# Kernel optimization log

Measured on AMD Instinct MI355X. Metric: run time of the kernel, lower is better.

## Reference

```python
import jax, jax.numpy as jnp
import numpy as np

P = 3  # patchsize
EMB = 1024  # pretrain/target embed dimension


def adaptive_avg_pool1d(x, T):
    """torch.F.adaptive_avg_pool1d over last axis (static boundaries)."""
    L = x.shape[-1]
    i = np.arange(T)
    starts = (i * L) // T
    ends = -((-(i + 1) * L) // T)  # ceil((i+1)*L/T)
    cs = jnp.cumsum(x, axis=-1)
    cs = jnp.concatenate([jnp.zeros(x.shape[:-1] + (1,), x.dtype), cs], axis=-1)
    return (cs[..., ends] - cs[..., starts]) / jnp.asarray(ends - starts, x.dtype)


def patchify(x):
    """nn.Unfold(kernel=3, stride=1, pad=1): [B,C,H,W] -> [B,H*W,C,3,3]."""
    B, C, H, W = x.shape
    xp = jnp.pad(x, ((0, 0), (0, 0), (1, 1), (1, 1)))
    pats = jnp.stack([xp[:, :, i:i + H, j:j + W] for i in range(P) for j in range(P)], axis=2)
    pats = pats.reshape(B, C, P, P, H * W).transpose(0, 4, 1, 2, 3)
    return pats, (H, W)


def embed(feat2, feat3):
    B = feat2.shape[0]
    f2, (h0, w0) = patchify(feat2)   # [B, h0*w0, 512, 3, 3]
    f3, (h1, w1) = patchify(feat3)   # [B, h1*w1, 1024, 3, 3]
    C3 = feat3.shape[1]
    # align layer3 patch grid to layer2 grid (bilinear, align_corners=False)
    f3 = f3.reshape(B, h1, w1, C3, P, P).transpose(0, 3, 4, 5, 1, 2)
    f3 = f3.reshape(-1, h1, w1)
    f3 = jax.image.resize(f3, (f3.shape[0], h0, w0), method='bilinear')
    f3 = f3.reshape(B, C3, P, P, h0, w0).transpose(0, 4, 5, 1, 2, 3)
    f3 = f3.reshape(B, h0 * w0, C3, P, P)
    # Preprocessing: MeanMapper per layer -> [N, 2, 1024]
    feats = []
    for f in (f2, f3):
        flat = f.reshape(-1, 1, f.shape[-3] * P * P)       # [N, 1, C*9]
        feats.append(adaptive_avg_pool1d(flat, EMB)[:, 0, :])
    x = jnp.stack(feats, axis=1)                           # [N, 2, 1024]
    # Aggregator: adaptive pool over flattened [N, 1, 2048] -> [N, 1024]
    x = adaptive_avg_pool1d(x.reshape(x.shape[0], 1, -1), EMB)[:, 0, :]
    return x, (h0, w0)


def setup_inputs() -> dict:
    key = jax.random.key(0)
    k1, k2, k3 = jax.random.split(key, 3)
    feat2 = jax.random.normal(k1, (8, 512, 28, 28), dtype=jnp.float32)
    feat3 = jax.random.normal(k2, (8, 1024, 14, 14), dtype=jnp.float32)
    memory_bank = jax.random.normal(k3, (16384, 1024), dtype=jnp.float32)
    return {"feat2": feat2, "feat3": feat3, "memory_bank": memory_bank}


def reference(feat2, feat3, memory_bank):
    B = feat2.shape[0]
    q, (h0, w0) = embed(feat2, feat3)                      # [B*h0*w0, 1024]
    # squared-L2 1-NN against the memory bank (faiss IndexFlatL2, k=1)
    d2 = (jnp.sum(q * q, axis=-1, keepdims=True)
          - 2.0 * (q @ memory_bank.T)
          + jnp.sum(memory_bank * memory_bank, axis=-1)[None, :])
    patch_scores = jnp.min(d2, axis=-1).reshape(B, h0, w0)  # unpatch_scores
    image_scores = jnp.max(patch_scores.reshape(B, -1), axis=-1)  # PatchMaker.score
    return image_scores, patch_scores
```

## Files before the change

### kernel.cpp

```cpp
#include <hip/hip_runtime.h>
#include <hip/hip_bf16.h>

typedef signed char i8;
typedef unsigned char u8;
typedef unsigned short u16;
typedef unsigned int u32;
typedef __attribute__((ext_vector_type(4))) int i32x4;

#define GLD16(g, l) __builtin_amdgcn_global_load_lds((const __attribute__((address_space(1))) u32*)(g), (__attribute__((address_space(3))) u32*)(l), 16, 0, 0)

#define SB (4.5f / 127.f)
#define SQ (2.0f / 127.f)
#define INV_SB (127.f / 4.5f)
#define INV_SQ (127.f / 2.0f)
#define TWO_S (2.0f * SB * SQ)

__device__ __forceinline__ u32 flipf(float f) {
    u32 u = __float_as_uint(f);
    return (u >> 31) ? ~u : (u | 0x80000000u);
}

__device__ __forceinline__ float unflipf(u32 k) {
    return __uint_as_float((k >> 31) ? (k ^ 0x80000000u) : ~k);
}

__device__ __forceinline__ int q8(float x, float invs) {
    return __float2int_rn(fminf(fmaxf(x * invs, -127.f), 127.f));
}

__device__ __forceinline__ void taps(int o, int& i0, int& i1, float& w0, float& w1) {
    int k = (o - 1) >> 1;
    float fy = (0.5f * (float)o - 0.25f) - (float)k;
    i0 = k; i1 = k + 1;
    w0 = 1.0f - fy; w1 = fy;
    if (i0 < 0)  { i0 = 0;  w0 = 0.0f; w1 = 1.0f; }
    if (i1 > 13) { i1 = 13; w1 = 0.0f; w0 = 1.0f; }
}

__global__ __launch_bounds__(256) void u_init_kernel(
    const float* __restrict__ f3, float* __restrict__ U,
    u32* __restrict__ minkey, float* __restrict__ qn2) {
    int bid = blockIdx.x, tid = threadIdx.x;
    if (bid < 25) {
        int i = bid * 256 + tid;
        if (i < 6400) minkey[i] = 0xFFFFFFFFu;
        if (i < 6272) qn2[i] = 0.f;
    }
    int idx = bid * 256 + tid;
    if (idx >= 8 * 512 * 196) return;
    int b = idx / (512 * 196);
    int rem = idx % (512 * 196);
    int t = rem / 196;
    int yx = rem % 196;
    int y = yx / 14, x = yx % 14;
    const float* p0 = f3 + ((size_t)(b * 1024 + 2 * t)) * 196;
    const float* p1 = p0 + 196;
    float s = 0.f;
    #pragma unroll
    for (int dy = -1; dy <= 1; ++dy) {
        int yy = y + dy; if ((unsigned)yy >= 14u) continue;
        #pragma unroll
        for (int dx = -1; dx <= 1; ++dx) {
            int xx = x + dx; if ((unsigned)xx >= 14u) continue;
            s += p0[yy * 14 + xx] + p1[yy * 14 + xx];
        }
    }
    U[idx] = s;
}

__global__ __launch_bounds__(256) void mbq_kernel(
    const float* __restrict__ mb, u8* __restrict__ mbb, float* __restrict__ mb2,
    const float* __restrict__ feat2, const float* __restrict__ U,
    u8* __restrict__ qb, float* __restrict__ qn2) {
    __shared__ float lds[3 * 64 * 29];
    const int bid0 = blockIdx.x;
    const int tid = threadIdx.x;

    if (bid0 >= 3584) {
        const int mrow = bid0 - 3584;
        float4 v = ((const float4*)(mb + (size_t)mrow * 1024))[tid];
        u32 p = ((u32)(u8)(i8)q8(v.x, INV_SB))
              | ((u32)(u8)(i8)q8(v.y, INV_SB) << 8)
              | ((u32)(u8)(i8)q8(v.z, INV_SB) << 16)
              | ((u32)(u8)(i8)q8(v.w, INV_SB) << 24);
        ((u32*)(mbb + (size_t)mrow * 1024))[tid] = p;
        float ssq = v.x * v.x + v.y * v.y + v.z * v.z + v.w * v.w;
        for (int s = 32; s; s >>= 1) ssq += __shfl_down(ssq, s);
        if ((tid & 63) == 0) lds[tid >> 6] = ssq;
        __syncthreads();
        if (tid == 0) mb2[mrow] = lds[0] + lds[1] + lds[2] + lds[3];
        return;
    }

    const int bid = bid0;
    const int b = bid / (28 * 16);
    const int rem = bid % (28 * 16);
    const int h = rem / 16;
    const int chunk = rem % 16;
    const int lane = tid & 63;
    const int wg = tid >> 6;

    if (chunk < 8) {
        const int c0 = chunk * 64;
        for (int i = tid; i < 3 * 64 * 28; i += 256) {
            int r = i / 1792;
            int rr = i % 1792;
            int c = rr / 28, x = rr % 28;
            int y = h - 1 + r;
            lds[(r * 64 + c) * 29 + x] = ((unsigned)y < 28u)
                ? feat2[((size_t)(b * 512 + c0 + c) * 28 + y) * 28 + x] : 0.f;
        }
        __syncthreads();
        const float* rowp = &lds[lane * 29];
        #pragma unroll
        for (int wi = 0; wi < 7; ++wi) {
            const int w = wg * 7 + wi;
            float s = 0.f;
            #pragma unroll
            for (int r = 0; r < 3; ++r) {
                #pragma unroll
                for (int dx = -1; dx <= 1; ++dx) {
                    int x = w + dx;
                    if ((unsigned)x >= 28u) continue;
                    float wt = (r == 1 && dx == 0) ? 2.f : 1.f;
                    s += wt * rowp[r * 64 * 29 + x];
                }
            }
            float val = s * 0.1f;
            const int n = b * 784 + h * 28 + w;
            qb[(size_t)n * 1024 + c0 + lane] = (u8)(i8)q8(val, INV_SQ);
            float ss = val * val;
            for (int sft = 32; sft; sft >>= 1) ss += __shfl_down(ss, sft);
            if (lane == 0) atomicAdd(&qn2[n], ss);
        }
    } else {
        const int t0 = (chunk - 8) * 64;
        int y0, y1; float wy0, wy1;
        taps(h, y0, y1, wy0, wy1);
        for (int i = tid; i < 2 * 64 * 14; i += 256) {
            int r = i / 896;
            int rr = i % 896;
            int t = rr / 14, x = rr % 14;
            lds[(r * 64 + t) * 15 + x] =
                U[(size_t)(b * 512 + t0 + t) * 196 + (r ? y1 : y0) * 14 + x];
        }
        __syncthreads();
        const float* rp0 = &lds[lane * 15];
        const float* rp1 = &lds[(64 + lane) * 15];
        #pragma unroll
        for (int wi = 0; wi < 7; ++wi) {
            const int w = wg * 7 + wi;
            int x0, x1; float wx0, wx1;
            taps(w, x0, x1, wx0, wx1);
            float val = (wy0 * (wx0 * rp0[x0] + wx1 * rp0[x1])
                       + wy1 * (wx0 * rp1[x0] + wx1 * rp1[x1])) * (1.f / 18.f);
            const int n = b * 784 + h * 28 + w;
            qb[(size_t)n * 1024 + 512 + t0 + lane] = (u8)(i8)q8(val, INV_SQ);
            float ss = val * val;
            for (int sft = 32; sft; sft >>= 1) ss += __shfl_down(ss, sft);
            if (lane == 0) atomicAdd(&qn2[n], ss);
        }
    }
}

__global__ __launch_bounds__(512, 4) void gemm_min_kernel(
    const u8* __restrict__ qb, const u8* __restrict__ mbb,
    const float* __restrict__ qn2, const float* __restrict__ mb2,
    u32* __restrict__ minkeys) {
    __shared__ __align__(16) u8 As[2][8192];
    __shared__ __align__(16) u8 Bs[2][16384];
    __shared__ u32 rowmin[128];

    const int tid = threadIdx.x;
    const int wid = tid >> 6;
    const int lane = tid & 63;
    const int wm = wid >> 2;
    const int wn = wid & 3;

    const int flat = blockIdx.x;
    const int swz = (flat & 7) * 400 + (flat >> 3);
    const int q0 = (swz % 50) * 128;
    const int m0 = (swz / 50) * 256;

    const int rloc = wid * 16 + (lane >> 2);
    const int sslot = (lane & 3) ^ ((lane >> 3) & 3);
    const size_t gA  = (size_t)(q0 + rloc) * 1024 + sslot * 16;
    const size_t gB0 = (size_t)(m0 + rloc) * 1024 + sslot * 16;
    const size_t gB1 = (size_t)(m0 + 128 + rloc) * 1024 + sslot * 16;
    const u32 ldA = wid * 1024;
    const u32 ldB1 = 8192 + wid * 1024;

    #define STAGE(T) { const int _t = (T); \
        GLD16(qb + gA + _t * 64, &As[_t & 1][ldA]); \
        GLD16(mbb + gB0 + _t * 64, &Bs[_t & 1][ldA]); \
        GLD16(mbb + gB1 + _t * 64, &Bs[_t & 1][ldB1]); }

    const u32 arow = (u32)(wm * 64 + (lane & 15)) * 64;
    const u32 brow = (u32)(wn * 64 + (lane & 15)) * 64;
    const u32 sl = (u32)(((lane >> 4) ^ (((lane & 15) >> 1) & 3)) * 16);

    i32x4 acc[4][4] = {};
    i32x4 a[4], b[4];

    STAGE(0);
    asm volatile("s_waitcnt vmcnt(0)" ::: "memory");
    __builtin_amdgcn_s_barrier();
    __builtin_amdgcn_sched_barrier(0);

    for (int t = 0; t < 16; ++t) {
        const u8* Ab = &As[t & 1][0];
        const u8* Bb = &Bs[t & 1][0];

        #pragma unroll
        for (int m = 0; m < 4; ++m) a[m] = *(const i32x4*)&Ab[arow + m * 1024 + sl];
        #pragma unroll
        for (int n = 0; n < 4; ++n) b[n] = *(const i32x4*)&Bb[brow + n * 1024 + sl];

        if (t < 15) STAGE(t + 1)

        asm volatile("s_waitcnt lgkmcnt(2)" ::: "memory");
        __builtin_amdgcn_sched_barrier(0);
        __builtin_amdgcn_s_setprio(1);
        #pragma unroll
        for (int m = 0; m < 4; ++m)
            #pragma unroll
            for (int n = 0; n < 2; ++n)
                acc[m][n] = __builtin_amdgcn_mfma_i32_16x16x64_i8(a[m], b[n], acc[m][n], 0, 0, 0);
        __builtin_amdgcn_s_setprio(0);
        asm volatile("s_waitcnt lgkmcnt(0)" ::: "memory");
        __builtin_amdgcn_sched_barrier(0);
        __builtin_amdgcn_s_setprio(1);
        #pragma unroll
        for (int m = 0; m < 4; ++m)
            #pragma unroll
            for (int n = 2; n < 4; ++n)
                acc[m][n] = __builtin_amdgcn_mfma_i32_16x16x64_i8(a[m], b[n], acc[m][n], 0, 0, 0);
        __builtin_amdgcn_s_setprio(0);

        if (t < 15) { asm volatile("s_waitcnt vmcnt(0)" ::: "memory"); }
        __builtin_amdgcn_s_barrier();
        __builtin_amdgcn_sched_barrier(0);
    }

    if (tid < 128) rowmin[tid] = 0xFFFFFFFFu;
    __syncthreads();

    float mb2v[4];
    #pragma unroll
    for (int n = 0; n < 4; ++n) mb2v[n] = mb2[m0 + wn * 64 + n * 16 + (lane & 15)];

    #pragma unroll
    for (int m = 0; m < 4; ++m) {
        #pragma unroll
        for (int r = 0; r < 4; ++r) {
            const int qrow = wm * 64 + m * 16 + (lane >> 4) * 4 + r;
            const float qq = qn2[q0 + qrow];
            float v = 3.4e38f;
            #pragma unroll
            for (int n = 0; n < 4; ++n) {
                float d2 = qq + mb2v[n] - TWO_S * (float)acc[m][n][r];
                v = fminf(v, d2);
            }
            #pragma unroll
            for (int s = 1; s < 16; s <<= 1) v = fminf(v, __shfl_xor(v, s));
            if ((lane & 15) == 0) atomicMin(&rowmin[qrow], flipf(v));
        }
    }
    __syncthreads();
    if (tid < 128) atomicMin(minkeys + q0 + tid, rowmin[tid]);
}

__global__ __launch_bounds__(256) void final_kernel(const u32* __restrict__ keys, float* __restrict__ out) {
    int b = blockIdx.x, tid = threadIdx.x;
    float mx = -3.4e38f;
    for (int i = tid; i < 784; i += 256) {
        float f = unflipf(keys[b * 784 + i]);
        out[8 + b * 784 + i] = f;
        mx = fmaxf(mx, f);
    }
    for (int s = 32; s; s >>= 1) mx = fmaxf(mx, __shfl_down(mx, s));
    __shared__ float sm[4];
    if ((tid & 63) == 0) sm[tid >> 6] = mx;
    __syncthreads();
    if (tid == 0) out[b] = fmaxf(fmaxf(sm[0], sm[1]), fmaxf(sm[2], sm[3]));
}

extern "C" void kernel_launch(void* const* d_in, const int* in_sizes, int n_in,
                              void* d_out, int out_size, void* d_ws, size_t ws_size,
                              hipStream_t stream) {
    const float* feat2 = (const float*)d_in[0];
    const float* feat3 = (const float*)d_in[1];
    const float* mb    = (const float*)d_in[2];
    float* out = (float*)d_out;

    char* ws = (char*)d_ws;
    float* U      = (float*)(ws);
    u8*    qb     = (u8*)   (ws + 3211264);
    u8*    mbb    = (u8*)   (ws + 9764864);
    float* qn2    = (float*)(ws + 26542080);
    float* mb2    = (float*)(ws + 26567168);
    u32*   minkey = (u32*)  (ws + 26632704);

    u_init_kernel<<<3136, 256, 0, stream>>>(feat3, U, minkey, qn2);
    mbq_kernel<<<19968, 256, 0, stream>>>(mb, mbb, mb2, feat2, U, qb, qn2);
    gemm_min_kernel<<<3200, 512, 0, stream>>>(qb, mbb, qn2, mb2, minkey);
    final_kernel<<<8, 256, 0, stream>>>(minkey, out);
}
```

Before: 183.8 us.

## Fuse layer3 box-sum into quantize kernel and final reduce into GEMM tail

Drops the separate U precompute kernel. The 3x3 channel-pair box sum of feat3 is now computed inside mbq_kernel from rows staged in LDS, which removes a global intermediate and one launch. The final max/unpatch kernel is also merged into gemm_min_kernel through a last-block-done atomic counter. This cuts launches and global traffic, but the layer3 blocks now load 4 rows of 128 channels per block, redoing work shared with neighbouring blocks, and LDS use grows.

```diff
diff --git a/kernel.cpp b/kernel.cpp
--- a/kernel.cpp
+++ b/kernel.cpp
@@ -37,42 +37,19 @@
     if (i1 > 13) { i1 = 13; w1 = 0.0f; w0 = 1.0f; }
 }
 
-__global__ __launch_bounds__(256) void u_init_kernel(
-    const float* __restrict__ f3, float* __restrict__ U,
-    u32* __restrict__ minkey, float* __restrict__ qn2) {
-    int bid = blockIdx.x, tid = threadIdx.x;
-    if (bid < 25) {
-        int i = bid * 256 + tid;
-        if (i < 6400) minkey[i] = 0xFFFFFFFFu;
-        if (i < 6272) qn2[i] = 0.f;
-    }
-    int idx = bid * 256 + tid;
-    if (idx >= 8 * 512 * 196) return;
-    int b = idx / (512 * 196);
-    int rem = idx % (512 * 196);
-    int t = rem / 196;
-    int yx = rem % 196;
-    int y = yx / 14, x = yx % 14;
-    const float* p0 = f3 + ((size_t)(b * 1024 + 2 * t)) * 196;
-    const float* p1 = p0 + 196;
-    float s = 0.f;
-    #pragma unroll
-    for (int dy = -1; dy <= 1; ++dy) {
-        int yy = y + dy; if ((unsigned)yy >= 14u) continue;
-        #pragma unroll
-        for (int dx = -1; dx <= 1; ++dx) {
-            int xx = x + dx; if ((unsigned)xx >= 14u) continue;
-            s += p0[yy * 14 + xx] + p1[yy * 14 + xx];
-        }
-    }
-    U[idx] = s;
+__global__ __launch_bounds__(256) void init_kernel(
+    u32* __restrict__ minkey, float* __restrict__ qn2, u32* __restrict__ counter) {
+    int i = blockIdx.x * 256 + threadIdx.x;
+    if (i < 6400) minkey[i] = 0xFFFFFFFFu;
+    if (i < 6272) qn2[i] = 0.f;
+    if (i == 0) *counter = 0;
 }
 
 __global__ __launch_bounds__(256) void mbq_kernel(
     const float* __restrict__ mb, u8* __restrict__ mbb, float* __restrict__ mb2,
-    const float* __restrict__ feat2, const float* __restrict__ U,
+    const float* __restrict__ feat2, const float* __restrict__ f3,
     u8* __restrict__ qb, float* __restrict__ qn2) {
-    __shared__ float lds[3 * 64 * 29];
+    __shared__ float lds[9600];
     const int bid0 = blockIdx.x;
     const int tid = threadIdx.x;
 
@@ -137,16 +114,44 @@
         const int t0 = (chunk - 8) * 64;
         int y0, y1; float wy0, wy1;
         taps(h, y0, y1, wy0, wy1);
-        for (int i = tid; i < 2 * 64 * 14; i += 256) {
-            int r = i / 896;
-            int rr = i % 896;
-            int t = rr / 14, x = rr % 14;
-            lds[(r * 64 + t) * 15 + x] =
-                U[(size_t)(b * 512 + t0 + t) * 196 + (r ? y1 : y0) * 14 + x];
+        const int rowbase = y0 - 1;
+        float* L3 = lds;
+        float* L2 = lds + 7680;
+        const float* f3b = f3 + (size_t)(b * 1024 + 2 * t0) * 196;
+        for (int i = tid; i < 4 * 128 * 14; i += 256) {
+            int r = i / 1792;
+            int rr = i % 1792;
+            int c = rr / 14, x = rr % 14;
+            int y = rowbase + r;
+            L3[(r * 128 + c) * 15 + x] = ((unsigned)y < 14u)
+                ? f3b[(size_t)c * 196 + y * 14 + x] : 0.f;
         }
         __syncthreads();
-        const float* rp0 = &lds[lane * 15];
-        const float* rp1 = &lds[(64 + lane) * 15];
+        {
+            const int t = tid & 63;
+            #pragma unroll
+            for (int k = 0; k < 7; ++k) {
+                int p = wg * 7 + k;
+                int yf = p / 14, x = p % 14;
+                int o = yf ? (y1 - y0) : 0;
+                float s = 0.f;
+                #pragma unroll
+                for (int dr = 0; dr < 3; ++dr) {
+                    const float* row0 = &L3[((o + dr) * 128 + 2 * t) * 15];
+                    const float* row1 = row0 + 15;
+                    #pragma unroll
+                    for (int dx = -1; dx <= 1; ++dx) {
+                        int xx = x + dx;
+                        if ((unsigned)xx >= 14u) continue;
+                        s += row0[xx] + row1[xx];
+                    }
+                }
+                L2[(yf * 64 + t) * 15 + x] = s;
+            }
+        }
+        __syncthreads();
+        const float* rp0 = &L2[lane * 15];
+        const float* rp1 = &L2[(64 + lane) * 15];
         #pragma unroll
         for (int wi = 0; wi < 7; ++wi) {
             const int w = wg * 7 + wi;
@@ -166,7 +171,7 @@
 __global__ __launch_bounds__(512, 4) void gemm_min_kernel(
     const u8* __restrict__ qb, const u8* __restrict__ mbb,
     const float* __restrict__ qn2, const float* __restrict__ mb2,
-    u32* __restrict__ minkeys) {
+    u32* __restrict__ minkeys, u32* __restrict__ counter, float* __restrict__ out) {
     __shared__ __align__(16) u8 As[2][8192];
     __shared__ __align__(16) u8 Bs[2][16384];
     __shared__ u32 rowmin[128];
@@ -268,21 +273,32 @@
     }
     __syncthreads();
     if (tid < 128) atomicMin(minkeys + q0 + tid, rowmin[tid]);
-}
-
-__global__ __launch_bounds__(256) void final_kernel(const u32* __restrict__ keys, float* __restrict__ out) {
-    int b = blockIdx.x, tid = threadIdx.x;
-    float mx = -3.4e38f;
-    for (int i = tid; i < 784; i += 256) {
-        float f = unflipf(keys[b * 784 + i]);
-        out[8 + b * 784 + i] = f;
-        mx = fmaxf(mx, f);
-    }
-    for (int s = 32; s; s >>= 1) mx = fmaxf(mx, __shfl_down(mx, s));
-    __shared__ float sm[4];
-    if ((tid & 63) == 0) sm[tid >> 6] = mx;
+
     __syncthreads();
-    if (tid == 0) out[b] = fmaxf(fmaxf(sm[0], sm[1]), fmaxf(sm[2], sm[3]));
+    __shared__ u32 lastf;
+    if (tid == 0) lastf = (atomicAdd(counter, 1) == 3199u) ? 1u : 0u;
+    __syncthreads();
+    if (lastf) {
+        __shared__ u32 smx[8];
+        for (int bb = 0; bb < 8; ++bb) {
+            u32 mk = 0;
+            for (int i = tid; i < 784; i += 512) {
+                u32 k = atomicMin(&minkeys[bb * 784 + i], 0xFFFFFFFFu);
+                out[8 + bb * 784 + i] = unflipf(k);
+                mk = mk > k ? mk : k;
+            }
+            for (int s = 32; s; s >>= 1) { u32 o = __shfl_down(mk, s); mk = mk > o ? mk : o; }
+            if ((tid & 63) == 0) smx[tid >> 6] = mk;
+            __syncthreads();
+            if (tid == 0) {
+                u32 m = smx[0];
+                #pragma unroll
+                for (int w = 1; w < 8; ++w) m = m > smx[w] ? m : smx[w];
+                out[bb] = unflipf(m);
+            }
+            __syncthreads();
+        }
+    }
 }
 
 extern "C" void kernel_launch(void* const* d_in, const int* in_sizes, int n_in,
@@ -294,15 +310,14 @@
     float* out = (float*)d_out;
 
     char* ws = (char*)d_ws;
-    float* U      = (float*)(ws);
-    u8*    qb     = (u8*)   (ws + 3211264);
-    u8*    mbb    = (u8*)   (ws + 9764864);
-    float* qn2    = (float*)(ws + 26542080);
-    float* mb2    = (float*)(ws + 26567168);
-    u32*   minkey = (u32*)  (ws + 26632704);
-
-    u_init_kernel<<<3136, 256, 0, stream>>>(feat3, U, minkey, qn2);
-    mbq_kernel<<<19968, 256, 0, stream>>>(mb, mbb, mb2, feat2, U, qb, qn2);
-    gemm_min_kernel<<<3200, 512, 0, stream>>>(qb, mbb, qn2, mb2, minkey);
-    final_kernel<<<8, 256, 0, stream>>>(minkey, out);
-}
+    u8*    qb     = (u8*)   (ws);
+    u8*    mbb    = (u8*)   (ws + 6553600);
+    float* qn2    = (float*)(ws + 23330816);
+    float* mb2    = (float*)(ws + 23355904);
+    u32*   minkey = (u32*)  (ws + 23421440);
+    u32*   counter= (u32*)  (ws + 23447040);
+
+    init_kernel<<<25, 256, 0, stream>>>(minkey, qn2, counter);
+    mbq_kernel<<<19968, 256, 0, stream>>>(mb, mbb, mb2, feat2, feat3, qb, qn2);
+    gemm_min_kernel<<<3200, 512, 0, stream>>>(qb, mbb, qn2, mb2, minkey, counter, out);
+}
```

Result: slower. 217.7 us (+18.4%).
